# Kernel tuning notes

Measured on AMD Instinct MI355X. Metric: run time of the kernel, lower is better.

Reference implementation:

```python
import math
import jax, jax.numpy as jnp
import numpy as np

BH, S, DK = 64, 1024, 64   # batch*heads, seq_len, head dim
FG, FL = 32, 32            # global / local enrichment feature dims
H, B = 16, 4               # mask layout [heads, batch, seq]


def setup_inputs() -> dict:
    key = jax.random.key(0)
    k1, k2, k3, k4, k5, k6 = jax.random.split(key, 6)
    return {
        "query": jax.random.normal(k1, (BH, S, DK), dtype=jnp.float32),
        "key": jax.random.normal(k2, (BH, S, DK), dtype=jnp.float32),
        "value": jax.random.normal(k3, (BH, S, DK), dtype=jnp.float32),
        "local_f": jax.random.normal(k4, (BH, S, FL), dtype=jnp.float32),
        "global_f": jax.random.normal(k5, (BH, S, FG), dtype=jnp.float32),
        "mask": jax.random.randint(k6, (H, B, S), 0, 2, dtype=jnp.int32),
    }


def reference(query, key, value, local_f, global_f, mask):
    dk = query.shape[-1]
    # enrich q/k with global then local features (matches torch concat order)
    pq = jnp.concatenate([query, global_f, local_f], axis=2)   # [BH, S, dk+fg+fl]
    pk = jnp.concatenate([key, global_f, local_f], axis=2)
    scores = jnp.einsum("bqd,bkd->bqk", pq, pk) / math.sqrt(dk)  # [BH, S, S]
    # mask [H, B, S] -> [H*B, S] -> broadcast over query positions
    m = mask.reshape(-1, mask.shape[-1])[:, None, :]            # [H*B, 1, S]
    scores = jnp.where(m == 1, jnp.float32(-1e9), scores)
    attn = jax.nn.softmax(scores, axis=-1)
    return jnp.einsum("bqk,bkd->bqd", attn, value)              # [BH, S, dk]
```

## Files before the change

### kernel.cpp

```cpp
#include <hip/hip_runtime.h>
#include <hip/hip_bf16.h>


#define BHn 64
#define Sn  1024
#define NT  16
#define KSTR 152
#define VSTR 72
#define KTILE (64*KSTR*2)
#define VTILE (64*VSTR*2)
#define BUFSZ (KTILE+VTILE)
#define OSTR 68
#define WAIT_VM0 0x0F70

typedef __attribute__((ext_vector_type(8)))  __bf16 bf16x8;
typedef __attribute__((ext_vector_type(16))) float  f32x16;
typedef __attribute__((ext_vector_type(4)))  unsigned int u32x4;

__device__ __forceinline__ unsigned f2bf1(float a){
    union { float f; unsigned u; } c; c.f = a;
    return (c.u + 0x7fffu + ((c.u >> 16) & 1u)) >> 16;
}
__device__ __forceinline__ unsigned f2bf2(float a, float b){
    return f2bf1(a) | (f2bf1(b) << 16);
}
__device__ __forceinline__ unsigned pkbf(float a, float b){
    return __builtin_amdgcn_perm(__builtin_bit_cast(unsigned, b),
                                 __builtin_bit_cast(unsigned, a), 0x07060302u);
}
__device__ __forceinline__ void gld_lds16(const void* g, void* l){
    __builtin_amdgcn_global_load_lds(
        (const __attribute__((address_space(1))) unsigned int*)g,
        (__attribute__((address_space(3))) unsigned int*)l, 16, 0, 0);
}

__global__ __launch_bounds__(256)
void attn_prep(const float* __restrict__ K, const float* __restrict__ V,
               const float* __restrict__ LF, const float* __restrict__ GF,
               const int* __restrict__ M,
               unsigned short* __restrict__ Kp, unsigned short* __restrict__ Vp)
{
    __shared__ __align__(16) unsigned char plds[BUFSZ];
    unsigned short* kl = (unsigned short*)plds;
    unsigned int*   vl = (unsigned int*)(plds + KTILE);

    const int tid = threadIdx.x;
    const int bh = blockIdx.x >> 4, ti = blockIdx.x & 15, kb = ti*64;

    #pragma unroll
    for (int i=0;i<2;i++){
        int idx = tid + 256*i, row = idx>>3, c = idx&7;
        const float* s = K + ((size_t)bh*Sn + kb + row)*64 + c*8;
        float4 f0 = *(const float4*)s, f1 = *(const float4*)(s+4);
        u32x4 w; w[0]=f2bf2(f0.x,f0.y); w[1]=f2bf2(f0.z,f0.w);
        w[2]=f2bf2(f1.x,f1.y); w[3]=f2bf2(f1.z,f1.w);
        *(u32x4*)(kl + row*KSTR + c*8) = w;
    }
    {
        int row = tid>>2, c = tid&3;
        const float* s = GF + ((size_t)bh*Sn + kb + row)*32 + c*8;
        float4 f0 = *(const float4*)s, f1 = *(const float4*)(s+4);
        u32x4 w; w[0]=f2bf2(f0.x,f0.y); w[1]=f2bf2(f0.z,f0.w);
        w[2]=f2bf2(f1.x,f1.y); w[3]=f2bf2(f1.z,f1.w);
        *(u32x4*)(kl + row*KSTR + 64 + c*8) = w;
    }
    {
        int row = tid>>2, c = tid&3;
        const float* s = LF + ((size_t)bh*Sn + kb + row)*32 + c*8;
        float4 f0 = *(const float4*)s, f1 = *(const float4*)(s+4);
        u32x4 w; w[0]=f2bf2(f0.x,f0.y); w[1]=f2bf2(f0.z,f0.w);
        w[2]=f2bf2(f1.x,f1.y); w[3]=f2bf2(f1.z,f1.w);
        *(u32x4*)(kl + row*KSTR + 96 + c*8) = w;
    }
    if (tid < 64){
        int mv = M[(size_t)bh*Sn + kb + tid];
        u32x4 w; w[0] = (mv == 1) ? 0x0000ceacu : 0u;
        w[1]=0u; w[2]=0u; w[3]=0u;
        *(u32x4*)(kl + tid*KSTR + 128) = w;
        u32x4 z; z[0]=0u; z[1]=0u; z[2]=0u; z[3]=0u;
        *(u32x4*)(kl + tid*KSTR + 136) = z;
        *(u32x4*)(kl + tid*KSTR + 144) = z;
    }
    {
        int d = tid & 63, g = tid >> 6;
        const float* vb = V + ((size_t)bh*Sn + kb + 16*g)*64 + d;
        const int pm[16] = {0,1,2,3, 8,9,10,11, 4,5,6,7, 12,13,14,15};
        unsigned w[8];
        #pragma unroll
        for (int m=0;m<8;m++)
            w[m] = f2bf2(vb[(size_t)pm[2*m]*64], vb[(size_t)pm[2*m+1]*64]);
        u32x4 a, b;
        a[0]=w[0]; a[1]=w[1]; a[2]=w[2]; a[3]=w[3];
        b[0]=w[4]; b[1]=w[5]; b[2]=w[6]; b[3]=w[7];
        *(u32x4*)(vl + d*36 + g*8)     = a;
        *(u32x4*)(vl + d*36 + g*8 + 4) = b;
        u32x4 z; z[0]=0u; z[1]=0u; z[2]=0u; z[3]=0u;
        *(u32x4*)(vl + d*36 + 32) = z;
    }
    __syncthreads();

    unsigned char* dK = (unsigned char*)Kp + (size_t)(bh*NT + ti)*KTILE;
    unsigned char* dV = (unsigned char*)Vp + (size_t)(bh*NT + ti)*VTILE;
    #pragma unroll
    for (int i=0;i<4;i++){
        int off = tid*16 + i*4096;
        *(u32x4*)(dK + off) = *(const u32x4*)(plds + off);
    }
    {
        int off = tid*16 + 4*4096;
        if (off < KTILE) *(u32x4*)(dK + off) = *(const u32x4*)(plds + off);
    }
    #pragma unroll
    for (int i=0;i<2;i++){
        int off = tid*16 + i*4096;
        *(u32x4*)(dV + off) = *(const u32x4*)(plds + KTILE + off);
    }
    {
        int off = tid*16 + 2*4096;
        if (off < VTILE) *(u32x4*)(dV + off) = *(const u32x4*)(plds + KTILE + off);
    }
}

__global__ __launch_bounds__(256, 2)
void attn_main(const float* __restrict__ Q, const unsigned short* __restrict__ Kp,
               const unsigned short* __restrict__ Vp,
               const float* __restrict__ GF, const float* __restrict__ LF,
               float* __restrict__ O)
{
    __shared__ __align__(16) unsigned char smem[2*BUFSZ];
    const int tid  = threadIdx.x;
    const int wave = tid >> 6, lane = tid & 63;
    const int l31  = lane & 31, h = lane >> 5;
    const int qp   = wave >> 1;
    const int kp   = wave & 1;
    const int bh = blockIdx.x & 63;
    const int qb = blockIdx.x >> 6;
    const float SCL = 0.18033688011112042f;

    u32x4 qf[2][8];
    #pragma unroll
    for (int sub = 0; sub < 2; sub++){
        const int qrow = qb*128 + qp*64 + sub*32 + l31;
        #pragma unroll
        for (int dc = 0; dc < 8; dc++){
            const int cb = dc*16 + 8*h;
            const float* src;
            if (cb < 64)      src = Q  + ((size_t)bh*Sn + qrow)*64 + cb;
            else if (cb < 96) src = GF + ((size_t)bh*Sn + qrow)*32 + (cb - 64);
            else              src = LF + ((size_t)bh*Sn + qrow)*32 + (cb - 96);
            float4 f0 = *(const float4*)src;
            float4 f1 = *(const float4*)(src + 4);
            qf[sub][dc][0] = f2bf2(f0.x*SCL, f0.y*SCL);
            qf[sub][dc][1] = f2bf2(f0.z*SCL, f0.w*SCL);
            qf[sub][dc][2] = f2bf2(f1.x*SCL, f1.y*SCL);
            qf[sub][dc][3] = f2bf2(f1.z*SCL, f1.w*SCL);
        }
    }
    u32x4 qfb;
    qfb[0] = h ? 0u : 0x00003f80u;
    qfb[1] = 0u; qfb[2] = 0u; qfb[3] = 0u;

    f32x16 oacc[2][2];
    #pragma unroll
    for (int sub=0; sub<2; sub++)
        #pragma unroll
        for (int dt=0; dt<2; dt++)
            #pragma unroll
            for (int r=0; r<16; r++) oacc[sub][dt][r] = 0.f;
    float lrun0 = 0.f, lrun1 = 0.f;

    const unsigned char* gKb = (const unsigned char*)Kp + (size_t)bh*NT*KTILE;
    const unsigned char* gVb = (const unsigned char*)Vp + (size_t)bh*NT*VTILE;

    #pragma unroll
    for (int i=0;i<7;i++){
        int c = wave + 4*i;
        if (c < 19) gld_lds16(gKb + (size_t)c*1024 + lane*16, smem + c*1024);
        else        gld_lds16(gVb + (size_t)(c-19)*1024 + lane*16,
                              smem + KTILE + (size_t)(c-19)*1024);
    }
    __builtin_amdgcn_s_waitcnt(WAIT_VM0);

    for (int t = 0; t < NT; t++){
        unsigned char* cur = smem + (size_t)(t&1)*BUFSZ;
        unsigned char* nxt = smem + (size_t)((t+1)&1)*BUFSZ;
        __syncthreads();
        if (t+1 < NT){
            const unsigned char* gK = gKb + (size_t)(t+1)*KTILE;
            const unsigned char* gV = gVb + (size_t)(t+1)*VTILE;
            #pragma unroll
            for (int i=0;i<7;i++){
                int c = wave + 4*i;
                if (c < 19) gld_lds16(gK + (size_t)c*1024 + lane*16, nxt + c*1024);
                else        gld_lds16(gV + (size_t)(c-19)*1024 + lane*16,
                                      nxt + KTILE + (size_t)(c-19)*1024);
            }
        }
        unsigned short* kt_s = (unsigned short*)cur;
        unsigned short* vt_s = (unsigned short*)(cur + KTILE);

        f32x16 acc0, acc1;
        #pragma unroll
        for (int r=0;r<16;r++){ acc0[r] = 0.f; acc1[r] = 0.f; }
        __builtin_amdgcn_s_setprio(1);
        #pragma unroll
        for (int dc=0; dc<8; dc++){
            u32x4 ar = *(const u32x4*)(kt_s + (kp*32 + l31)*KSTR + dc*16 + 8*h);
            acc0 = __builtin_amdgcn_mfma_f32_32x32x16_bf16(
                    __builtin_bit_cast(bf16x8, ar),
                    __builtin_bit_cast(bf16x8, qf[0][dc]), acc0, 0, 0, 0);
            acc1 = __builtin_amdgcn_mfma_f32_32x32x16_bf16(
                    __builtin_bit_cast(bf16x8, ar),
                    __builtin_bit_cast(bf16x8, qf[1][dc]), acc1, 0, 0, 0);
        }
        {
            u32x4 ab = *(const u32x4*)(kt_s + (kp*32 + l31)*KSTR + 128 + 8*h);
            acc0 = __builtin_amdgcn_mfma_f32_32x32x16_bf16(
                    __builtin_bit_cast(bf16x8, ab),
                    __builtin_bit_cast(bf16x8, qfb), acc0, 0, 0, 0);
            acc1 = __builtin_amdgcn_mfma_f32_32x32x16_bf16(
                    __builtin_bit_cast(bf16x8, ab),
                    __builtin_bit_cast(bf16x8, qfb), acc1, 0, 0, 0);
        }
        __builtin_amdgcn_s_setprio(0);

        float rs0 = 0.f, rs1 = 0.f;
        #pragma unroll
        for (int r=0;r<16;r++){
            float p0 = __builtin_amdgcn_exp2f(acc0[r]);
            float p1 = __builtin_amdgcn_exp2f(acc1[r]);
            acc0[r] = p0; rs0 += p0;
            acc1[r] = p1; rs1 += p1;
        }
        lrun0 += rs0; lrun1 += rs1;

        unsigned pk0[8], pk1[8];
        #pragma unroll
        for (int i=0;i<8;i++){
            pk0[i] = pkbf(acc0[2*i], acc0[2*i+1]);
            pk1[i] = pkbf(acc1[2*i], acc1[2*i+1]);
        }
        u32x4 b00, b01, b10, b11;
        b00[0]=pk0[0]; b00[1]=pk0[1]; b00[2]=pk0[2]; b00[3]=pk0[3];
        b01[0]=pk0[4]; b01[1]=pk0[5]; b01[2]=pk0[6]; b01[3]=pk0[7];
        b10[0]=pk1[0]; b10[1]=pk1[1]; b10[2]=pk1[2]; b10[3]=pk1[3];
        b11[0]=pk1[4]; b11[1]=pk1[5]; b11[2]=pk1[6]; b11[3]=pk1[7];

        __builtin_amdgcn_s_setprio(1);
        #pragma unroll
        for (int dt=0;dt<2;dt++){
            u32x4 va0 = *(const u32x4*)(vt_s + (dt*32 + l31)*VSTR + kp*32 + 8*h);
            u32x4 va1 = *(const u32x4*)(vt_s + (dt*32 + l31)*VSTR + kp*32 + 16 + 8*h);
            oacc[0][dt] = __builtin_amdgcn_mfma_f32_32x32x16_bf16(
                    __builtin_bit_cast(bf16x8, va0),
                    __builtin_bit_cast(bf16x8, b00), oacc[0][dt], 0, 0, 0);
            oacc[0][dt] = __builtin_amdgcn_mfma_f32_32x32x16_bf16(
                    __builtin_bit_cast(bf16x8, va1),
                    __builtin_bit_cast(bf16x8, b01), oacc[0][dt], 0, 0, 0);
            oacc[1][dt] = __builtin_amdgcn_mfma_f32_32x32x16_bf16(
                    __builtin_bit_cast(bf16x8, va0),
                    __builtin_bit_cast(bf16x8, b10), oacc[1][dt], 0, 0, 0);
            oacc[1][dt] = __builtin_amdgcn_mfma_f32_32x32x16_bf16(
                    __builtin_bit_cast(bf16x8, va1),
                    __builtin_bit_cast(bf16x8, b11), oacc[1][dt], 0, 0, 0);
        }
        __builtin_amdgcn_s_setprio(0);

        __builtin_amdgcn_s_waitcnt(WAIT_VM0);
    }

    __syncthreads();
    float lw0 = lrun0 + __shfl_xor(lrun0, 32, 64);
    float lw1 = lrun1 + __shfl_xor(lrun1, 32, 64);
    float* s1 = (float*)smem;
    float* s2 = (float*)(smem + 128*OSTR*4);
    if (kp == 1){
        #pragma unroll
        for (int sub=0;sub<2;sub++)
            #pragma unroll
            for (int dt=0;dt<2;dt++)
                #pragma unroll
                for (int rg=0;rg<4;rg++){
                    float4 w;
                    w.x = oacc[sub][dt][rg*4+0]; w.y = oacc[sub][dt][rg*4+1];
                    w.z = oacc[sub][dt][rg*4+2]; w.w = oacc[sub][dt][rg*4+3];
                    *(float4*)(s1 + (qp*64 + sub*32 + l31)*OSTR + dt*32 + rg*8 + 4*h) = w;
                }
        if (h == 0){
            s2[qp*64 + l31]      = lw0;
            s2[qp*64 + 32 + l31] = lw1;
        }
    }
    __syncthreads();
    if (kp == 0){
        float inv0 = 1.0f / (lw0 + s2[qp*64 + l31]);
        float inv1 = 1.0f / (lw1 + s2[qp*64 + 32 + l31]);
        #pragma unroll
        for (int sub=0;sub<2;sub++){
            float inv = sub ? inv1 : inv0;
            #pragma unroll
            for (int dt=0;dt<2;dt++)
                #pragma unroll
                for (int rg=0;rg<4;rg++){
                    float* p = s1 + (qp*64 + sub*32 + l31)*OSTR + dt*32 + rg*8 + 4*h;
                    float4 w = *(float4*)p;
                    w.x = (w.x + oacc[sub][dt][rg*4+0])*inv;
                    w.y = (w.y + oacc[sub][dt][rg*4+1])*inv;
                    w.z = (w.z + oacc[sub][dt][rg*4+2])*inv;
                    w.w = (w.w + oacc[sub][dt][rg*4+3])*inv;
                    *(float4*)p = w;
                }
        }
    }
    __syncthreads();
    #pragma unroll
    for (int i=0;i<8;i++){
        int idx = tid + 256*i, r = idx>>4, c = idx&15;
        *(float4*)(O + ((size_t)bh*Sn + qb*128 + r)*64 + c*4) =
            *(const float4*)(s1 + r*OSTR + c*4);
    }
}

extern "C" void kernel_launch(void* const* d_in, const int* in_sizes, int n_in,
                              void* d_out, int out_size, void* d_ws, size_t ws_size,
                              hipStream_t stream) {
    const float* Q  = (const float*)d_in[0];
    const float* K  = (const float*)d_in[1];
    const float* V  = (const float*)d_in[2];
    const float* LF = (const float*)d_in[3];
    const float* GF = (const float*)d_in[4];
    const int*   M  = (const int*)d_in[5];
    float* O = (float*)d_out;

    unsigned short* Kp = (unsigned short*)d_ws;
    unsigned short* Vp = Kp + (size_t)BHn*NT*64*KSTR;

    attn_prep<<<dim3(BHn*NT), dim3(256), 0, stream>>>(K, V, LF, GF, M, Kp, Vp);
    attn_main<<<dim3(BHn*(Sn/128)), dim3(256), 0, stream>>>(Q, Kp, Vp, GF, LF, O);
}
```

Before: 144.3 us.

## Software-pipeline QK of next tile with softmax and PV of current

```diff
diff --git a/kernel.cpp b/kernel.cpp
--- a/kernel.cpp
+++ b/kernel.cpp
@@ -119,6 +119,44 @@
         int off = tid*16 + 2*4096;
         if (off < VTILE) *(u32x4*)(dV + off) = *(const u32x4*)(plds + KTILE + off);
     }
+}
+
+__device__ __forceinline__ void stage_tile(const unsigned char* gK,
+                                           const unsigned char* gV,
+                                           unsigned char* dst,
+                                           int wave, int lane){
+    #pragma unroll
+    for (int i=0;i<7;i++){
+        int c = wave + 4*i;
+        if (c < 19) gld_lds16(gK + (size_t)c*1024 + lane*16, dst + c*1024);
+        else        gld_lds16(gV + (size_t)(c-19)*1024 + lane*16,
+                              dst + KTILE + (size_t)(c-19)*1024);
+    }
+}
+
+__device__ __forceinline__ void qk_step(const unsigned short* kt_s,
+                                        int kp, int l31, int h,
+                                        const u32x4 (&qf)[2][8], const u32x4& qfb,
+                                        f32x16& a0, f32x16& a1){
+    #pragma unroll
+    for (int r=0;r<16;r++){ a0[r] = 0.f; a1[r] = 0.f; }
+    #pragma unroll
+    for (int dc=0; dc<8; dc++){
+        u32x4 ar = *(const u32x4*)(kt_s + (kp*32 + l31)*KSTR + dc*16 + 8*h);
+        a0 = __builtin_amdgcn_mfma_f32_32x32x16_bf16(
+                __builtin_bit_cast(bf16x8, ar),
+                __builtin_bit_cast(bf16x8, qf[0][dc]), a0, 0, 0, 0);
+        a1 = __builtin_amdgcn_mfma_f32_32x32x16_bf16(
+                __builtin_bit_cast(bf16x8, ar),
+                __builtin_bit_cast(bf16x8, qf[1][dc]), a1, 0, 0, 0);
+    }
+    u32x4 ab = *(const u32x4*)(kt_s + (kp*32 + l31)*KSTR + 128 + 8*h);
+    a0 = __builtin_amdgcn_mfma_f32_32x32x16_bf16(
+            __builtin_bit_cast(bf16x8, ab),
+            __builtin_bit_cast(bf16x8, qfb), a0, 0, 0, 0);
+    a1 = __builtin_amdgcn_mfma_f32_32x32x16_bf16(
+            __builtin_bit_cast(bf16x8, ab),
+            __builtin_bit_cast(bf16x8, qfb), a1, 0, 0, 0);
 }
 
 __global__ __launch_bounds__(256, 2)
@@ -137,6 +175,11 @@
     const int qb = blockIdx.x >> 6;
     const float SCL = 0.18033688011112042f;
 
+    const unsigned char* gKb = (const unsigned char*)Kp + (size_t)bh*NT*KTILE;
+    const unsigned char* gVb = (const unsigned char*)Vp + (size_t)bh*NT*VTILE;
+
+    stage_tile(gKb, gVb, smem, wave, lane);
+
     u32x4 qf[2][8];
     #pragma unroll
     for (int sub = 0; sub < 2; sub++){
@@ -169,76 +212,49 @@
             for (int r=0; r<16; r++) oacc[sub][dt][r] = 0.f;
     float lrun0 = 0.f, lrun1 = 0.f;
 
-    const unsigned char* gKb = (const unsigned char*)Kp + (size_t)bh*NT*KTILE;
-    const unsigned char* gVb = (const unsigned char*)Vp + (size_t)bh*NT*VTILE;
-
-    #pragma unroll
-    for (int i=0;i<7;i++){
-        int c = wave + 4*i;
-        if (c < 19) gld_lds16(gKb + (size_t)c*1024 + lane*16, smem + c*1024);
-        else        gld_lds16(gVb + (size_t)(c-19)*1024 + lane*16,
-                              smem + KTILE + (size_t)(c-19)*1024);
-    }
     __builtin_amdgcn_s_waitcnt(WAIT_VM0);
-
+    __syncthreads();
+    stage_tile(gKb + KTILE, gVb + VTILE, smem + BUFSZ, wave, lane);
+    f32x16 as0, as1;
+    qk_step((const unsigned short*)smem, kp, l31, h, qf, qfb, as0, as1);
+
+    #pragma unroll 2
     for (int t = 0; t < NT; t++){
         unsigned char* cur = smem + (size_t)(t&1)*BUFSZ;
         unsigned char* nxt = smem + (size_t)((t+1)&1)*BUFSZ;
+        const unsigned short* vt_s = (const unsigned short*)(cur + KTILE);
+
+        u32x4 vr00 = *(const u32x4*)(vt_s + (     l31)*VSTR + kp*32 + 8*h);
+        u32x4 vr01 = *(const u32x4*)(vt_s + (     l31)*VSTR + kp*32 + 16 + 8*h);
+        u32x4 vr10 = *(const u32x4*)(vt_s + (32 + l31)*VSTR + kp*32 + 8*h);
+        u32x4 vr11 = *(const u32x4*)(vt_s + (32 + l31)*VSTR + kp*32 + 16 + 8*h);
+
+        __builtin_amdgcn_s_waitcnt(WAIT_VM0);
         __syncthreads();
-        if (t+1 < NT){
-            const unsigned char* gK = gKb + (size_t)(t+1)*KTILE;
-            const unsigned char* gV = gVb + (size_t)(t+1)*VTILE;
-            #pragma unroll
-            for (int i=0;i<7;i++){
-                int c = wave + 4*i;
-                if (c < 19) gld_lds16(gK + (size_t)c*1024 + lane*16, nxt + c*1024);
-                else        gld_lds16(gV + (size_t)(c-19)*1024 + lane*16,
-                                      nxt + KTILE + (size_t)(c-19)*1024);
-            }
-        }
-        unsigned short* kt_s = (unsigned short*)cur;
-        unsigned short* vt_s = (unsigned short*)(cur + KTILE);
-
-        f32x16 acc0, acc1;
-        #pragma unroll
-        for (int r=0;r<16;r++){ acc0[r] = 0.f; acc1[r] = 0.f; }
+
+        if (t+2 < NT)
+            stage_tile(gKb + (size_t)(t+2)*KTILE, gVb + (size_t)(t+2)*VTILE,
+                       cur, wave, lane);
+
         __builtin_amdgcn_s_setprio(1);
-        #pragma unroll
-        for (int dc=0; dc<8; dc++){
-            u32x4 ar = *(const u32x4*)(kt_s + (kp*32 + l31)*KSTR + dc*16 + 8*h);
-            acc0 = __builtin_amdgcn_mfma_f32_32x32x16_bf16(
-                    __builtin_bit_cast(bf16x8, ar),
-                    __builtin_bit_cast(bf16x8, qf[0][dc]), acc0, 0, 0, 0);
-            acc1 = __builtin_amdgcn_mfma_f32_32x32x16_bf16(
-                    __builtin_bit_cast(bf16x8, ar),
-                    __builtin_bit_cast(bf16x8, qf[1][dc]), acc1, 0, 0, 0);
-        }
-        {
-            u32x4 ab = *(const u32x4*)(kt_s + (kp*32 + l31)*KSTR + 128 + 8*h);
-            acc0 = __builtin_amdgcn_mfma_f32_32x32x16_bf16(
-                    __builtin_bit_cast(bf16x8, ab),
-                    __builtin_bit_cast(bf16x8, qfb), acc0, 0, 0, 0);
-            acc1 = __builtin_amdgcn_mfma_f32_32x32x16_bf16(
-                    __builtin_bit_cast(bf16x8, ab),
-                    __builtin_bit_cast(bf16x8, qfb), acc1, 0, 0, 0);
-        }
-        __builtin_amdgcn_s_setprio(0);
-
-        float rs0 = 0.f, rs1 = 0.f;
+        float p0[16], p1[16];
         #pragma unroll
         for (int r=0;r<16;r++){
-            float p0 = __builtin_amdgcn_exp2f(acc0[r]);
-            float p1 = __builtin_amdgcn_exp2f(acc1[r]);
-            acc0[r] = p0; rs0 += p0;
-            acc1[r] = p1; rs1 += p1;
-        }
-        lrun0 += rs0; lrun1 += rs1;
-
+            p0[r] = __builtin_amdgcn_exp2f(as0[r]);
+            p1[r] = __builtin_amdgcn_exp2f(as1[r]);
+        }
+        float s0[8], s1[8];
+        #pragma unroll
+        for (int r=0;r<8;r++){ s0[r] = p0[2*r] + p0[2*r+1]; s1[r] = p1[2*r] + p1[2*r+1]; }
+        #pragma unroll
+        for (int r=0;r<4;r++){ s0[r] = s0[2*r] + s0[2*r+1]; s1[r] = s1[2*r] + s1[2*r+1]; }
+        lrun0 += (s0[0]+s0[1]) + (s0[2]+s0[3]);
+        lrun1 += (s1[0]+s1[1]) + (s1[2]+s1[3]);
         unsigned pk0[8], pk1[8];
         #pragma unroll
         for (int i=0;i<8;i++){
-            pk0[i] = pkbf(acc0[2*i], acc0[2*i+1]);
-            pk1[i] = pkbf(acc1[2*i], acc1[2*i+1]);
+            pk0[i] = pkbf(p0[2*i], p0[2*i+1]);
+            pk1[i] = pkbf(p1[2*i], p1[2*i+1]);
         }
         u32x4 b00, b01, b10, b11;
         b00[0]=pk0[0]; b00[1]=pk0[1]; b00[2]=pk0[2]; b00[3]=pk0[3];
@@ -246,34 +262,44 @@
         b10[0]=pk1[0]; b10[1]=pk1[1]; b10[2]=pk1[2]; b10[3]=pk1[3];
         b11[0]=pk1[4]; b11[1]=pk1[5]; b11[2]=pk1[6]; b11[3]=pk1[7];
 
-        __builtin_amdgcn_s_setprio(1);
-        #pragma unroll
-        for (int dt=0;dt<2;dt++){
-            u32x4 va0 = *(const u32x4*)(vt_s + (dt*32 + l31)*VSTR + kp*32 + 8*h);
-            u32x4 va1 = *(const u32x4*)(vt_s + (dt*32 + l31)*VSTR + kp*32 + 16 + 8*h);
-            oacc[0][dt] = __builtin_amdgcn_mfma_f32_32x32x16_bf16(
-                    __builtin_bit_cast(bf16x8, va0),
-                    __builtin_bit_cast(bf16x8, b00), oacc[0][dt], 0, 0, 0);
-            oacc[0][dt] = __builtin_amdgcn_mfma_f32_32x32x16_bf16(
-                    __builtin_bit_cast(bf16x8, va1),
-                    __builtin_bit_cast(bf16x8, b01), oacc[0][dt], 0, 0, 0);
-            oacc[1][dt] = __builtin_amdgcn_mfma_f32_32x32x16_bf16(
-                    __builtin_bit_cast(bf16x8, va0),
-                    __builtin_bit_cast(bf16x8, b10), oacc[1][dt], 0, 0, 0);
-            oacc[1][dt] = __builtin_amdgcn_mfma_f32_32x32x16_bf16(
-                    __builtin_bit_cast(bf16x8, va1),
-                    __builtin_bit_cast(bf16x8, b11), oacc[1][dt], 0, 0, 0);
-        }
+        f32x16 an0, an1;
+        if (t+1 < NT)
+            qk_step((const unsigned short*)nxt, kp, l31, h, qf, qfb, an0, an1);
+
+        oacc[0][0] = __builtin_amdgcn_mfma_f32_32x32x16_bf16(
+                __builtin_bit_cast(bf16x8, vr00), __builtin_bit_cast(bf16x8, b00),
+                oacc[0][0], 0, 0, 0);
+        oacc[0][0] = __builtin_amdgcn_mfma_f32_32x32x16_bf16(
+                __builtin_bit_cast(bf16x8, vr01), __builtin_bit_cast(bf16x8, b01),
+                oacc[0][0], 0, 0, 0);
+        oacc[0][1] = __builtin_amdgcn_mfma_f32_32x32x16_bf16(
+                __builtin_bit_cast(bf16x8, vr10), __builtin_bit_cast(bf16x8, b00),
+                oacc[0][1], 0, 0, 0);
+        oacc[0][1] = __builtin_amdgcn_mfma_f32_32x32x16_bf16(
+                __builtin_bit_cast(bf16x8, vr11), __builtin_bit_cast(bf16x8, b01),
+                oacc[0][1], 0, 0, 0);
+        oacc[1][0] = __builtin_amdgcn_mfma_f32_32x32x16_bf16(
+                __builtin_bit_cast(bf16x8, vr00), __builtin_bit_cast(bf16x8, b10),
+                oacc[1][0], 0, 0, 0);
+        oacc[1][0] = __builtin_amdgcn_mfma_f32_32x32x16_bf16(
+                __builtin_bit_cast(bf16x8, vr01), __builtin_bit_cast(bf16x8, b11),
+                oacc[1][0], 0, 0, 0);
+        oacc[1][1] = __builtin_amdgcn_mfma_f32_32x32x16_bf16(
+                __builtin_bit_cast(bf16x8, vr10), __builtin_bit_cast(bf16x8, b10),
+                oacc[1][1], 0, 0, 0);
+        oacc[1][1] = __builtin_amdgcn_mfma_f32_32x32x16_bf16(
+                __builtin_bit_cast(bf16x8, vr11), __builtin_bit_cast(bf16x8, b11),
+                oacc[1][1], 0, 0, 0);
         __builtin_amdgcn_s_setprio(0);
 
-        __builtin_amdgcn_s_waitcnt(WAIT_VM0);
+        if (t+1 < NT){ as0 = an0; as1 = an1; }
     }
 
     __syncthreads();
     float lw0 = lrun0 + __shfl_xor(lrun0, 32, 64);
     float lw1 = lrun1 + __shfl_xor(lrun1, 32, 64);
-    float* s1 = (float*)smem;
-    float* s2 = (float*)(smem + 128*OSTR*4);
+    float* s1m = (float*)smem;
+    float* s2m = (float*)(smem + 128*OSTR*4);
     if (kp == 1){
         #pragma unroll
         for (int sub=0;sub<2;sub++)
@@ -284,17 +310,17 @@
                     float4 w;
                     w.x = oacc[sub][dt][rg*4+0]; w.y = oacc[sub][dt][rg*4+1];
                     w.z = oacc[sub][dt][rg*4+2]; w.w = oacc[sub][dt][rg*4+3];
-                    *(float4*)(s1 + (qp*64 + sub*32 + l31)*OSTR + dt*32 + rg*8 + 4*h) = w;
+                    *(float4*)(s1m + (qp*64 + sub*32 + l31)*OSTR + dt*32 + rg*8 + 4*h) = w;
                 }
         if (h == 0){
-            s2[qp*64 + l31]      = lw0;
-            s2[qp*64 + 32 + l31] = lw1;
+            s2m[qp*64 + l31]      = lw0;
+            s2m[qp*64 + 32 + l31] = lw1;
         }
     }
     __syncthreads();
     if (kp == 0){
-        float inv0 = 1.0f / (lw0 + s2[qp*64 + l31]);
-        float inv1 = 1.0f / (lw1 + s2[qp*64 + 32 + l31]);
+        float inv0 = 1.0f / (lw0 + s2m[qp*64 + l31]);
+        float inv1 = 1.0f / (lw1 + s2m[qp*64 + 32 + l31]);
         #pragma unroll
         for (int sub=0;sub<2;sub++){
             float inv = sub ? inv1 : inv0;
@@ -302,7 +328,7 @@
             for (int dt=0;dt<2;dt++)
                 #pragma unroll
                 for (int rg=0;rg<4;rg++){
-                    float* p = s1 + (qp*64 + sub*32 + l31)*OSTR + dt*32 + rg*8 + 4*h;
+                    float* p = s1m + (qp*64 + sub*32 + l31)*OSTR + dt*32 + rg*8 + 4*h;
                     float4 w = *(float4*)p;
                     w.x = (w.x + oacc[sub][dt][rg*4+0])*inv;
                     w.y = (w.y + oacc[sub][dt][rg*4+1])*inv;
@@ -317,7 +343,7 @@
     for (int i=0;i<8;i++){
         int idx = tid + 256*i, r = idx>>4, c = idx&15;
         *(float4*)(O + ((size_t)bh*Sn + qb*128 + r)*64 + c*4) =
-            *(const float4*)(s1 + r*OSTR + c*4);
+            *(const float4*)(s1m + r*OSTR + c*4);
     }
 }
 
```

Measured after the change: 168.5 us. +16.8%, slower.
